# Kernel optimization log

Hardware: AMD Instinct MI355X
Metric: run time of the kernel (lower is better)

The kernel has to match this reference:

```python
import jax, jax.numpy as jnp
import numpy as np

HIDDEN = 3584
NUM_HEADS = 28
NUM_KV_HEADS = 4
HEAD_DIM = 128
ROPE_THETA = 1000000.0
B, S = 2, 2048


def setup_inputs() -> dict:
    key = jax.random.key(0)
    k1, k2, k3, k4 = jax.random.split(key, 4)
    q_size = NUM_HEADS * HEAD_DIM
    kv_size = NUM_KV_HEADS * HEAD_DIM
    return {
        "positions": jnp.arange(B * S, dtype=jnp.int32).reshape(B, S),
        "hidden_states": jax.random.normal(k1, (B, S, HIDDEN), dtype=jnp.float32),
        "w_qkv": jax.random.normal(k2, (HIDDEN, q_size + 2 * kv_size), dtype=jnp.float32) * (HIDDEN ** -0.5),
        "b_qkv": jax.random.normal(k3, (q_size + 2 * kv_size,), dtype=jnp.float32) * 0.02,
        "w_o": jax.random.normal(k4, (q_size, HIDDEN), dtype=jnp.float32) * (q_size ** -0.5),
    }


def _rope_cos_sin(positions):
    # NeoX-style rotary embedding, rotary_dim == head_dim
    half = HEAD_DIM // 2
    inv_freq = 1.0 / (ROPE_THETA ** (jnp.arange(0, half, dtype=jnp.float32) * 2.0 / HEAD_DIM))
    angles = positions.astype(jnp.float32)[..., None] * inv_freq  # [B, S, half]
    return jnp.cos(angles), jnp.sin(angles)


def _apply_rope(x, cos, sin):
    # x: [B, S, H, D]; cos/sin: [B, S, half] -> broadcast over heads
    x1, x2 = jnp.split(x, 2, axis=-1)
    c = cos[:, :, None, :]
    s = sin[:, :, None, :]
    return jnp.concatenate([x1 * c - x2 * s, x2 * c + x1 * s], axis=-1)


def reference(positions, hidden_states, w_qkv, b_qkv, w_o):
    q_size = NUM_HEADS * HEAD_DIM
    kv_size = NUM_KV_HEADS * HEAD_DIM
    scaling = HEAD_DIM ** -0.5
    groups = NUM_HEADS // NUM_KV_HEADS

    qkv = hidden_states @ w_qkv + b_qkv  # [B, S, q+2kv]
    q, k, v = jnp.split(qkv, [q_size, q_size + kv_size], axis=-1)
    q = q.reshape(B, S, NUM_HEADS, HEAD_DIM)
    k = k.reshape(B, S, NUM_KV_HEADS, HEAD_DIM)
    v = v.reshape(B, S, NUM_KV_HEADS, HEAD_DIM)

    cos, sin = _rope_cos_sin(positions)
    q = _apply_rope(q, cos, sin)
    k = _apply_rope(k, cos, sin)

    # GQA: group query heads over kv heads. q: [B, S, Hkv, G, D]
    qg = q.reshape(B, S, NUM_KV_HEADS, groups, HEAD_DIM)
    scores = jnp.einsum("bqhgd,bkhd->bhgqk", qg, k) * scaling  # [B, Hkv, G, S, S]
    causal = jnp.tril(jnp.ones((S, S), dtype=bool))
    scores = jnp.where(causal, scores, jnp.finfo(scores.dtype).min)
    probs = jax.nn.softmax(scores, axis=-1)
    o = jnp.einsum("bhgqk,bkhd->bqhgd", probs, v)  # [B, S, Hkv, G, D]
    o = o.reshape(B, S, NUM_HEADS * HEAD_DIM)
    return o @ w_o  # [B, S, HIDDEN]
```

## Files before the change

kernel.cpp:

```cpp
#include <hip/hip_runtime.h>

typedef unsigned short u16;
typedef unsigned int u32;
typedef __bf16 bf16x8 __attribute__((ext_vector_type(8)));
typedef float f32x4 __attribute__((ext_vector_type(4)));

#define NHEAD 28
#define NKVH 4
#define HD 128
#define NB 2
#define NS 2048
#define NTOK 4096
#define HIDDEN_DIM 3584
#define QKVW 4608
#define QSZ 3584
#define KOFF 3584
#define VOFF 4096
#define VSLAB (NTOK * 512)
#define QSCALE_L2E 0.12751744f

__device__ __forceinline__ float bf2f(u16 u) {
  u32 x = ((u32)u) << 16; float f; __builtin_memcpy(&f, &x, 4); return f;
}
__device__ __forceinline__ u16 f2bf(float f) {
  u32 x; __builtin_memcpy(&x, &f, 4);
  x += 0x7FFFu + ((x >> 16) & 1u);
  return (u16)(x >> 16);
}
__device__ __forceinline__ u32 pack2bf(float a, float b) {
  __bf16 lo = (__bf16)a, hi = (__bf16)b;
  u16 ul, uh;
  __builtin_memcpy(&ul, &lo, 2); __builtin_memcpy(&uh, &hi, 2);
  return (u32)ul | ((u32)uh << 16);
}
__device__ __forceinline__ void async16(const void* g, void* lds) {
  __builtin_amdgcn_global_load_lds((const __attribute__((address_space(1))) void*)g,
                                   (__attribute__((address_space(3))) void*)lds,
                                   16, 0, 0);
}

#define SB __builtin_amdgcn_sched_barrier(0)
#define BAR do { SB; __builtin_amdgcn_s_barrier(); SB; } while (0)

__global__ void cast_f32_bf16(const float* __restrict__ in, u16* __restrict__ out) {
  int i = (blockIdx.x * 256 + threadIdx.x) * 4;
  float4 v = *(const float4*)(in + i);
  u32 p0 = (u32)f2bf(v.x) | ((u32)f2bf(v.y) << 16);
  u32 p1 = (u32)f2bf(v.z) | ((u32)f2bf(v.w) << 16);
  uint2 r; r.x = p0; r.y = p1;
  *(uint2*)(out + i) = r;
}

__global__ void transpose_cast(const float* __restrict__ in, u16* __restrict__ out,
                               int R, int C) {
  __shared__ float tile[32][33];
  int tx = threadIdx.x & 31, ty = threadIdx.x >> 5;
  int c0 = blockIdx.x * 32, r0 = blockIdx.y * 32;
#pragma unroll
  for (int i = 0; i < 32; i += 8)
    tile[ty + i][tx] = in[(size_t)(r0 + ty + i) * C + c0 + tx];
  __syncthreads();
#pragma unroll
  for (int i = 0; i < 32; i += 8)
    out[(size_t)(c0 + ty + i) * R + r0 + tx] = f2bf(tile[tx][ty + i]);
}

__global__ void rope_table(const int* __restrict__ positions,
                           float* __restrict__ cs, float* __restrict__ sn) {
  int idx = blockIdx.x * 256 + threadIdx.x;
  int t = idx >> 6, i = idx & 63;
  float p = (float)positions[t];
  float inv = expf(-(float)i * (13.815510557964274f / 64.f));
  float a = p * inv;
  cs[idx] = cosf(a);
  sn[idx] = sinf(a);
}

__global__ void rope_kernel(u16* __restrict__ qkv, const float* __restrict__ cs,
                            const float* __restrict__ sn) {
  int w = threadIdx.x >> 6, l = threadIdx.x & 63;
  int rid = blockIdx.x * 4 + w;
  int t = rid >> 5, hh = rid & 31;
  size_t base = (size_t)t * QKVW + (hh < NHEAD ? hh * HD : KOFF + (hh - NHEAD) * HD);
  float x1 = bf2f(qkv[base + l]), x2 = bf2f(qkv[base + l + 64]);
  float c = cs[t * 64 + l], s = sn[t * 64 + l];
  float y1 = x1 * c - x2 * s;
  float y2 = x2 * c + x1 * s;
  if (hh < NHEAD) { y1 *= QSCALE_L2E; y2 *= QSCALE_L2E; }
  qkv[base + l] = f2bf(y1);
  qkv[base + l + 64] = f2bf(y2);
}

template <int MODE>
__global__ __launch_bounds__(512, 2) void gemm256(
    const u16* __restrict__ A, const u16* __restrict__ Bt,
    const float* __restrict__ bias, u16* __restrict__ outb,
    float* __restrict__ outf, int M, int Next, int Kst, int ldc, int NT) {
  __shared__ __align__(16) u16 Al[2][256 * 64];
  __shared__ __align__(16) u16 Bl[2][256 * 64];
  const int tid = threadIdx.x;
  const int l = tid & 63, w = tid >> 6;
  const int g = l >> 4, r = l & 15;
  const int wm = w >> 2, wn = w & 3;
  const int nbx = Next >> 8;
  const int cpx = (int)gridDim.x >> 3;
  const int bid = ((int)blockIdx.x & 7) * cpx + ((int)blockIdx.x >> 3);
  int bx, by, kbase;
  float* outp = outf;
  if (MODE == 2) {
    const int tps = nbx * (M >> 8);
    const int ks = bid / tps, rem = bid % tps;
    by = rem / nbx; bx = rem % nbx;
    kbase = ks * (NT << 6);
    outp = outf + (size_t)ks * M * Next;
  } else {
    bx = bid % nbx; by = bid / nbx; kbase = 0;
  }
  const int row0 = by * 256, col0 = bx * 256;

  f32x4 acc[8][4] = {};
  bf16x8 af[4][2];
  bf16x8 bfr[2][2][2];

  auto stageU = [&](const u16* mb, int base0, char* ldsMat, int h, int t) {
#pragma unroll
    for (int q = 0; q < 2; ++q) {
      const int idx = q * 512 + tid;
      const int rho = h * 128 + (idx >> 3);
      const int sl = (idx & 7) ^ (rho & 7);
      async16(mb + (size_t)(base0 + rho) * Kst + kbase + t * 64 + sl * 8,
              ldsMat + (size_t)(t & 1) * 32768 + h * 16384 + idx * 16);
    }
  };

#define READ_A(s, rh)                                                           \
  _Pragma("unroll") for (int fr = 0; fr < 4; ++fr) {                            \
    const int row_ = (rh) * 128 + wm * 64 + fr * 16 + r;                        \
    _Pragma("unroll") for (int kk = 0; kk < 2; ++kk) {                          \
      const int sl_ = (kk * 4 + g) ^ (row_ & 7);                                \
      af[fr][kk] = *(const bf16x8*)((const char*)Al + (s) * 32768 +             \
                                    row_ * 128 + sl_ * 16);                     \
    }                                                                           \
  }
#define READ_B(s, ch)                                                           \
  _Pragma("unroll") for (int fc = 0; fc < 2; ++fc) {                            \
    const int col_ = (ch) * 128 + wn * 32 + fc * 16 + r;                        \
    _Pragma("unroll") for (int kk = 0; kk < 2; ++kk) {                          \
      const int sl_ = (kk * 4 + g) ^ (col_ & 7);                                \
      bfr[ch][fc][kk] = *(const bf16x8*)((const char*)Bl + (s) * 32768 +        \
                                         col_ * 128 + sl_ * 16);                \
    }                                                                           \
  }
#define MFMA_Q(rh, ch)                                                          \
  __builtin_amdgcn_s_setprio(1);                                                \
  _Pragma("unroll") for (int fr = 0; fr < 4; ++fr)                              \
  _Pragma("unroll") for (int fc = 0; fc < 2; ++fc)                              \
  _Pragma("unroll") for (int kk = 0; kk < 2; ++kk)                              \
    acc[(rh) * 4 + fr][(ch) * 2 + fc] = __builtin_amdgcn_mfma_f32_16x16x32_bf16( \
        af[fr][kk], bfr[ch][fc][kk], acc[(rh) * 4 + fr][(ch) * 2 + fc], 0, 0, 0);\
  __builtin_amdgcn_s_setprio(0);

  stageU(A, row0, (char*)Al, 0, 0); stageU(A, row0, (char*)Al, 1, 0);
  stageU(Bt, col0, (char*)Bl, 0, 0); stageU(Bt, col0, (char*)Bl, 1, 0);
  stageU(A, row0, (char*)Al, 0, 1); stageU(Bt, col0, (char*)Bl, 0, 1);
  SB; asm volatile("s_waitcnt vmcnt(4)" ::: "memory");
  BAR;

  for (int t = 0; t < NT; ++t) {
    const int s = t & 1;
    READ_A(s, 0); READ_B(s, 0);
    if (t + 1 < NT) stageU(A, row0, (char*)Al, 1, t + 1);
    BAR; MFMA_Q(0, 0); BAR;
    READ_B(s, 1);
    if (t + 1 < NT) stageU(Bt, col0, (char*)Bl, 1, t + 1);
    BAR; MFMA_Q(0, 1); BAR;
    READ_A(s, 1);
    if (t + 2 < NT) stageU(A, row0, (char*)Al, 0, t + 2);
    BAR; MFMA_Q(1, 0); BAR;
    if (t + 2 < NT) stageU(Bt, col0, (char*)Bl, 0, t + 2);
    BAR; MFMA_Q(1, 1);
    if (t < NT - 2)        { SB; asm volatile("s_waitcnt vmcnt(4)" ::: "memory"); }
    else if (t == NT - 2)  { SB; asm volatile("s_waitcnt vmcnt(0)" ::: "memory"); }
    BAR;
  }
  SB; asm volatile("s_waitcnt vmcnt(0)" ::: "memory");

#pragma unroll
  for (int m = 0; m < 8; ++m) {
    const int row = row0 + (m >> 2) * 128 + wm * 64 + (m & 3) * 16 + g * 4;
#pragma unroll
    for (int n = 0; n < 4; ++n) {
      const int col = col0 + (n >> 1) * 128 + wn * 32 + (n & 1) * 16 + r;
      const float bb = (MODE == 0) ? bias[col] : 0.f;
#pragma unroll
      for (int j = 0; j < 4; ++j) {
        float v = acc[m][n][j] + bb;
        if (MODE == 0) outb[(size_t)(row + j) * ldc + col] = f2bf(v);
        else           outp[(size_t)(row + j) * ldc + col] = v;
      }
    }
  }
}

__global__ void v_reduce(const float* __restrict__ slabs, const float* __restrict__ bias,
                         u16* __restrict__ vtg) {
  __shared__ float tile[32][33];
  const int tx = threadIdx.x & 31, ty = threadIdx.x >> 5;
  const int c0 = blockIdx.x * 32;
  const int r0 = blockIdx.y * 32;
#pragma unroll
  for (int i = 0; i < 32; i += 8) {
    const size_t idx = (size_t)(r0 + ty + i) * 512 + c0 + tx;
    float s = slabs[idx] + slabs[idx + VSLAB] + slabs[idx + 2 * VSLAB] +
              slabs[idx + 3 * VSLAB];
    tile[ty + i][tx] = s + bias[VOFF + c0 + tx];
  }
  __syncthreads();
#pragma unroll
  for (int i = 0; i < 32; i += 8) {
    const int col = c0 + ty + i;
    const int row = r0 + tx;
    vtg[((size_t)((((row >> 11) * NKVH) + (col >> 7)) * HD + (col & 127))) * NS +
        (row & 2047)] = f2bf(tile[tx][ty + i]);
  }
}

__global__ __launch_bounds__(512) void attn_kernel(const u16* __restrict__ qkv,
                                                   const u16* __restrict__ vtg,
                                                   u16* __restrict__ Oh) {
  __shared__ __align__(16) u16 Ks[2][64 * 128];
  __shared__ __align__(16) u16 Vt[128 * 64];
  const int tid = threadIdx.x, l = tid & 63, w = tid >> 6;
  const int g = l >> 4, r = l & 15;
  const int bidx = blockIdx.x;
  const int qt = 15 - (bidx & 15);
  const int bh = bidx >> 4;
  const int h = bh % NHEAD, b = bh / NHEAD;
  const int kvh = h / 7;
  const int q0 = qt * 128;

  const int qrow = q0 + w * 16 + r;
  const size_t qbase = (size_t)(b * NS + qrow) * QKVW + h * HD;
  bf16x8 qf[4];
#pragma unroll
  for (int ks = 0; ks < 4; ++ks)
    qf[ks] = *(const bf16x8*)(qkv + qbase + ks * 32 + g * 8);

  const u16* kb0 = qkv + (size_t)(b * NS) * QKVW + KOFF + kvh * HD;
  const u16* vb0 = vtg + (size_t)((b * NKVH + kvh) * HD) * NS;

  f32x4 oacc[8] = {};
  float mrun = -1e30f, lrun = 0.f;

  const int nkv = 2 * qt + 2;

  auto stageK = [&](u16* kdst, int kv0) {
#pragma unroll
    for (int i = 0; i < 2; ++i) {
      const int li = (w * 2 + i) * 64 + l;
      const int rr = li >> 4, c = li & 15;
      async16(kb0 + (size_t)(kv0 + rr) * QKVW + ((c ^ (rr & 7)) << 3),
              (char*)kdst + (w * 2 + i) * 1024);
    }
  };
  auto stageV = [&](int kv0) {
#pragma unroll
    for (int i = 0; i < 2; ++i) {
      const int li = (w * 2 + i) * 64 + l;
      const int d = li >> 3, c = li & 7;
      async16(vb0 + (size_t)d * NS + kv0 + ((c ^ (d & 7)) << 3),
              (char*)Vt + (w * 2 + i) * 1024);
    }
  };

  stageK(Ks[0], 0);
  int cur = 0;
  const int srcA = r + ((l & 16) << 1);
  const int srcB = srcA + 16;
  const bool hi = (l & 32) != 0;

  for (int kvt = 0; kvt < nkv; ++kvt) {
    const int kv0 = kvt * 64;
    asm volatile("s_waitcnt vmcnt(0) lgkmcnt(0)" ::: "memory");
    __builtin_amdgcn_s_barrier();
    __builtin_amdgcn_sched_barrier(0);

    stageV(kv0);
    const bool haveNext = (kvt + 1 < nkv);
    if (haveNext) stageK(Ks[cur ^ 1], kv0 + 64);

    const bool active = kv0 <= q0 + w * 16 + 15;

    union { u32 wrd[4]; bf16x8 v; } pf[2];
    if (active) {
      f32x4 sacc[4] = {};
      const char* ksB = (const char*)Ks[cur];
      __builtin_amdgcn_s_setprio(1);
#pragma unroll
      for (int n = 0; n < 4; ++n) {
        const int key = n * 16 + r;
        const int sw = (key & 7) << 4;
#pragma unroll
        for (int ks = 0; ks < 4; ++ks) {
          bf16x8 kf = *(const bf16x8*)(ksB + key * 256 + ((ks * 64 + g * 16) ^ sw));
          sacc[n] = __builtin_amdgcn_mfma_f32_16x16x32_bf16(kf, qf[ks], sacc[n], 0, 0, 0);
        }
      }
      __builtin_amdgcn_s_setprio(0);
      if (kv0 + 63 > q0 + w * 16) {
#pragma unroll
        for (int n = 0; n < 4; ++n) {
          const int key_g = kv0 + n * 16 + g * 4;
#pragma unroll
          for (int j = 0; j < 4; ++j)
            if (key_g + j > qrow) sacc[n][j] = -1e30f;
        }
      }
      float mx = fmaxf(fmaxf(sacc[0][0], sacc[0][1]), fmaxf(sacc[0][2], sacc[0][3]));
#pragma unroll
      for (int n = 1; n < 4; ++n)
        mx = fmaxf(mx, fmaxf(fmaxf(sacc[n][0], sacc[n][1]), fmaxf(sacc[n][2], sacc[n][3])));
      mx = fmaxf(mx, __shfl_xor(mx, 16, 64));
      mx = fmaxf(mx, __shfl_xor(mx, 32, 64));
      if (!__all(mx <= mrun + 8.0f)) {
        const float mnew = fmaxf(mrun, mx);
        const float scale = __builtin_amdgcn_exp2f(mrun - mnew);
        mrun = mnew;
        lrun *= scale;
#pragma unroll
        for (int dt = 0; dt < 8; ++dt) oacc[dt] *= scale;
      }
      float sum = 0.f;
#pragma unroll
      for (int n = 0; n < 4; ++n)
#pragma unroll
        for (int j = 0; j < 4; ++j) {
          float p = __builtin_amdgcn_exp2f(sacc[n][j] - mrun);
          sacc[n][j] = p;
          sum += p;
        }
      sum += __shfl_xor(sum, 16, 64);
      sum += __shfl_xor(sum, 32, 64);
      lrun += sum;

      u32 pk[4][2];
#pragma unroll
      for (int n = 0; n < 4; ++n) {
        pk[n][0] = pack2bf(sacc[n][0], sacc[n][1]);
        pk[n][1] = pack2bf(sacc[n][2], sacc[n][3]);
      }
#pragma unroll
      for (int ks2 = 0; ks2 < 2; ++ks2) {
        const int n0 = 2 * ks2, n1 = 2 * ks2 + 1;
#pragma unroll
        for (int hh2 = 0; hh2 < 2; ++hh2) {
          u32 a0 = (u32)__shfl((int)pk[n0][hh2], srcA, 64);
          u32 a1 = (u32)__shfl((int)pk[n1][hh2], srcA, 64);
          pf[ks2].wrd[hh2] = hi ? a1 : a0;
          u32 b0 = (u32)__shfl((int)pk[n0][hh2], srcB, 64);
          u32 b1 = (u32)__shfl((int)pk[n1][hh2], srcB, 64);
          pf[ks2].wrd[2 + hh2] = hi ? b1 : b0;
        }
      }
    }

    if (haveNext) asm volatile("s_waitcnt vmcnt(2)" ::: "memory");
    else          asm volatile("s_waitcnt vmcnt(0)" ::: "memory");
    __builtin_amdgcn_s_barrier();
    __builtin_amdgcn_sched_barrier(0);
    if (active) {
      const char* vtB = (const char*)Vt;
      __builtin_amdgcn_s_setprio(1);
#pragma unroll
      for (int ks2 = 0; ks2 < 2; ++ks2) {
#pragma unroll
        for (int dt = 0; dt < 8; ++dt) {
          const int d = dt * 16 + r;
          bf16x8 vf = *(const bf16x8*)(vtB + d * 128 +
                                       ((ks2 * 64 + g * 16) ^ ((d & 7) << 4)));
          oacc[dt] = __builtin_amdgcn_mfma_f32_16x16x32_bf16(vf, pf[ks2].v, oacc[dt], 0, 0, 0);
        }
      }
      __builtin_amdgcn_s_setprio(0);
    }
    cur ^= 1;
  }

  const float inv = 1.f / lrun;
  const size_t obase = (size_t)(b * NS + qrow) * QSZ + h * HD;
#pragma unroll
  for (int dt = 0; dt < 8; ++dt) {
    uint2 r2;
    r2.x = pack2bf(oacc[dt][0] * inv, oacc[dt][1] * inv);
    r2.y = pack2bf(oacc[dt][2] * inv, oacc[dt][3] * inv);
    *(uint2*)(Oh + obase + dt * 16 + 4 * g) = r2;
  }
}

extern "C" void kernel_launch(void* const* d_in, const int* in_sizes, int n_in,
                              void* d_out, int out_size, void* d_ws, size_t ws_size,
                              hipStream_t stream) {
  const int* positions = (const int*)d_in[0];
  const float* hidden = (const float*)d_in[1];
  const float* w_qkv = (const float*)d_in[2];
  const float* b_qkv = (const float*)d_in[3];
  const float* w_o = (const float*)d_in[4];
  float* out = (float*)d_out;

  char* ws = (char*)d_ws;
  const size_t XB_OFF = 0;
  const size_t WQT_OFF = 29360128;
  const size_t QKV_OFF = WQT_OFF + 33030144;
  const size_t CS_OFF = QKV_OFF + 37748736;
  const size_t SN_OFF = CS_OFF + 1048576;
  const size_t WS_NEED = SN_OFF + 1048576;
  if (ws_size < WS_NEED) return;

  u16* Xb = (u16*)(ws + XB_OFF);
  u16* WoT = (u16*)(ws + XB_OFF);
  u16* WqT = (u16*)(ws + WQT_OFF);
  u16* Oh = (u16*)(ws + WQT_OFF);
  u16* qkvb = (u16*)(ws + QKV_OFF);
  float* cs = (float*)(ws + CS_OFF);
  float* sn = (float*)(ws + SN_OFF);
  u16* vtg = (u16*)d_out;
  float* vslabs = (float*)((char*)d_out + 4194304);

  cast_f32_bf16<<<14336, 256, 0, stream>>>(hidden, Xb);
  transpose_cast<<<dim3(QKVW / 32, HIDDEN_DIM / 32), 256, 0, stream>>>(w_qkv, WqT, HIDDEN_DIM, QKVW);
  rope_table<<<(NTOK * 64) / 256, 256, 0, stream>>>(positions, cs, sn);

  gemm256<0><<<256, 512, 0, stream>>>(
      Xb, WqT, b_qkv, qkvb, nullptr, NTOK, 4096, HIDDEN_DIM, QKVW, HIDDEN_DIM / 64);

  gemm256<2><<<128, 512, 0, stream>>>(
      Xb, WqT + (size_t)VOFF * HIDDEN_DIM, nullptr, nullptr, vslabs,
      NTOK, 512, HIDDEN_DIM, 512, HIDDEN_DIM / 64 / 4);

  v_reduce<<<dim3(512 / 32, NTOK / 32), 256, 0, stream>>>(vslabs, b_qkv, vtg);

  rope_kernel<<<(NTOK * 32) / 4, 256, 0, stream>>>(qkvb, cs, sn);

  transpose_cast<<<dim3(HIDDEN_DIM / 32, QSZ / 32), 256, 0, stream>>>(w_o, WoT, QSZ, HIDDEN_DIM);

  attn_kernel<<<NB * NHEAD * (NS / 128), 512, 0, stream>>>(qkvb, vtg, Oh);

  gemm256<1><<<(HIDDEN_DIM / 256) * (NTOK / 256), 512, 0, stream>>>(
      Oh, WoT, nullptr, nullptr, out, NTOK, HIDDEN_DIM, QSZ, HIDDEN_DIM, QSZ / 64);
}
```

Measured before the change: 494.0 us.

## Make attention a persistent kernel with atomic job queue, heaviest tiles first

Attention blocks become persistent workers that pull (q-tile, batch, head) jobs from a global atomic counter. Jobs are ordered longest causal tile first, which load-balances the triangular work across CUs. The counter is reset inside the rope_table kernel. The per-iteration row-sum shuffle reduction is deferred to the end of each job, and the max shuffles now run only when a rescale happens. This adds an atomic plus a block barrier per job. Reusing LDS across jobs relies on the existing barriers for ordering.

```diff
diff --git a/kernel.cpp b/kernel.cpp
--- a/kernel.cpp
+++ b/kernel.cpp
@@ -17,6 +17,8 @@
 #define KOFF 3584
 #define VOFF 4096
 #define VSLAB (NTOK * 512)
+#define NJOBS 896
+#define ATTN_BLOCKS 768
 #define QSCALE_L2E 0.12751744f
 
 __device__ __forceinline__ float bf2f(u16 u) {
@@ -66,7 +68,9 @@
 }
 
 __global__ void rope_table(const int* __restrict__ positions,
-                           float* __restrict__ cs, float* __restrict__ sn) {
+                           float* __restrict__ cs, float* __restrict__ sn,
+                           int* __restrict__ ctr) {
+  if (blockIdx.x == 0 && threadIdx.x == 0) *ctr = 0;
   int idx = blockIdx.x * 256 + threadIdx.x;
   int t = idx >> 6, i = idx & 63;
   float p = (float)positions[t];
@@ -227,173 +231,181 @@
 
 __global__ __launch_bounds__(512) void attn_kernel(const u16* __restrict__ qkv,
                                                    const u16* __restrict__ vtg,
-                                                   u16* __restrict__ Oh) {
+                                                   u16* __restrict__ Oh,
+                                                   int* __restrict__ ctr) {
   __shared__ __align__(16) u16 Ks[2][64 * 128];
   __shared__ __align__(16) u16 Vt[128 * 64];
+  __shared__ int s_job;
   const int tid = threadIdx.x, l = tid & 63, w = tid >> 6;
   const int g = l >> 4, r = l & 15;
-  const int bidx = blockIdx.x;
-  const int qt = 15 - (bidx & 15);
-  const int bh = bidx >> 4;
-  const int h = bh % NHEAD, b = bh / NHEAD;
-  const int kvh = h / 7;
-  const int q0 = qt * 128;
-
-  const int qrow = q0 + w * 16 + r;
-  const size_t qbase = (size_t)(b * NS + qrow) * QKVW + h * HD;
-  bf16x8 qf[4];
-#pragma unroll
-  for (int ks = 0; ks < 4; ++ks)
-    qf[ks] = *(const bf16x8*)(qkv + qbase + ks * 32 + g * 8);
-
-  const u16* kb0 = qkv + (size_t)(b * NS) * QKVW + KOFF + kvh * HD;
-  const u16* vb0 = vtg + (size_t)((b * NKVH + kvh) * HD) * NS;
-
-  f32x4 oacc[8] = {};
-  float mrun = -1e30f, lrun = 0.f;
-
-  const int nkv = 2 * qt + 2;
-
-  auto stageK = [&](u16* kdst, int kv0) {
-#pragma unroll
-    for (int i = 0; i < 2; ++i) {
-      const int li = (w * 2 + i) * 64 + l;
-      const int rr = li >> 4, c = li & 15;
-      async16(kb0 + (size_t)(kv0 + rr) * QKVW + ((c ^ (rr & 7)) << 3),
-              (char*)kdst + (w * 2 + i) * 1024);
-    }
-  };
-  auto stageV = [&](int kv0) {
-#pragma unroll
-    for (int i = 0; i < 2; ++i) {
-      const int li = (w * 2 + i) * 64 + l;
-      const int d = li >> 3, c = li & 7;
-      async16(vb0 + (size_t)d * NS + kv0 + ((c ^ (d & 7)) << 3),
-              (char*)Vt + (w * 2 + i) * 1024);
-    }
-  };
-
-  stageK(Ks[0], 0);
-  int cur = 0;
   const int srcA = r + ((l & 16) << 1);
   const int srcB = srcA + 16;
   const bool hi = (l & 32) != 0;
 
-  for (int kvt = 0; kvt < nkv; ++kvt) {
-    const int kv0 = kvt * 64;
-    asm volatile("s_waitcnt vmcnt(0) lgkmcnt(0)" ::: "memory");
-    __builtin_amdgcn_s_barrier();
-    __builtin_amdgcn_sched_barrier(0);
-
-    stageV(kv0);
-    const bool haveNext = (kvt + 1 < nkv);
-    if (haveNext) stageK(Ks[cur ^ 1], kv0 + 64);
-
-    const bool active = kv0 <= q0 + w * 16 + 15;
-
-    union { u32 wrd[4]; bf16x8 v; } pf[2];
-    if (active) {
-      f32x4 sacc[4] = {};
-      const char* ksB = (const char*)Ks[cur];
-      __builtin_amdgcn_s_setprio(1);
-#pragma unroll
-      for (int n = 0; n < 4; ++n) {
-        const int key = n * 16 + r;
-        const int sw = (key & 7) << 4;
-#pragma unroll
-        for (int ks = 0; ks < 4; ++ks) {
-          bf16x8 kf = *(const bf16x8*)(ksB + key * 256 + ((ks * 64 + g * 16) ^ sw));
-          sacc[n] = __builtin_amdgcn_mfma_f32_16x16x32_bf16(kf, qf[ks], sacc[n], 0, 0, 0);
-        }
+  for (;;) {
+    if (tid == 0) s_job = atomicAdd(ctr, 1);
+    __syncthreads();
+    const int jid = s_job;
+    if (jid >= NJOBS) return;
+    const int qtr = jid / 56;
+    const int qt = 15 - qtr;
+    const int bh = jid - qtr * 56;
+    const int h = bh % NHEAD, b = bh / NHEAD;
+    const int kvh = h / 7;
+    const int q0 = qt * 128;
+
+    const int qrow = q0 + w * 16 + r;
+    const size_t qbase = (size_t)(b * NS + qrow) * QKVW + h * HD;
+    bf16x8 qf[4];
+#pragma unroll
+    for (int ks = 0; ks < 4; ++ks)
+      qf[ks] = *(const bf16x8*)(qkv + qbase + ks * 32 + g * 8);
+
+    const u16* kb0 = qkv + (size_t)(b * NS) * QKVW + KOFF + kvh * HD;
+    const u16* vb0 = vtg + (size_t)((b * NKVH + kvh) * HD) * NS;
+
+    f32x4 oacc[8] = {};
+    float mrun = -1e30f, lsum = 0.f;
+
+    const int nkv = 2 * qt + 2;
+
+    auto stageK = [&](u16* kdst, int kv0) {
+#pragma unroll
+      for (int i = 0; i < 2; ++i) {
+        const int li = (w * 2 + i) * 64 + l;
+        const int rr = li >> 4, c = li & 15;
+        async16(kb0 + (size_t)(kv0 + rr) * QKVW + ((c ^ (rr & 7)) << 3),
+                (char*)kdst + (w * 2 + i) * 1024);
       }
-      __builtin_amdgcn_s_setprio(0);
-      if (kv0 + 63 > q0 + w * 16) {
+    };
+    auto stageV = [&](int kv0) {
+#pragma unroll
+      for (int i = 0; i < 2; ++i) {
+        const int li = (w * 2 + i) * 64 + l;
+        const int d = li >> 3, c = li & 7;
+        async16(vb0 + (size_t)d * NS + kv0 + ((c ^ (d & 7)) << 3),
+                (char*)Vt + (w * 2 + i) * 1024);
+      }
+    };
+
+    stageK(Ks[0], 0);
+    int cur = 0;
+
+    for (int kvt = 0; kvt < nkv; ++kvt) {
+      const int kv0 = kvt * 64;
+      asm volatile("s_waitcnt vmcnt(0) lgkmcnt(0)" ::: "memory");
+      __builtin_amdgcn_s_barrier();
+      __builtin_amdgcn_sched_barrier(0);
+
+      stageV(kv0);
+      const bool haveNext = (kvt + 1 < nkv);
+      if (haveNext) stageK(Ks[cur ^ 1], kv0 + 64);
+
+      const bool active = kv0 <= q0 + w * 16 + 15;
+
+      union { u32 wrd[4]; bf16x8 v; } pf[2];
+      if (active) {
+        f32x4 sacc[4] = {};
+        const char* ksB = (const char*)Ks[cur];
+        __builtin_amdgcn_s_setprio(1);
 #pragma unroll
         for (int n = 0; n < 4; ++n) {
-          const int key_g = kv0 + n * 16 + g * 4;
-#pragma unroll
-          for (int j = 0; j < 4; ++j)
-            if (key_g + j > qrow) sacc[n][j] = -1e30f;
+          const int key = n * 16 + r;
+          const int sw = (key & 7) << 4;
+#pragma unroll
+          for (int ks = 0; ks < 4; ++ks) {
+            bf16x8 kf = *(const bf16x8*)(ksB + key * 256 + ((ks * 64 + g * 16) ^ sw));
+            sacc[n] = __builtin_amdgcn_mfma_f32_16x16x32_bf16(kf, qf[ks], sacc[n], 0, 0, 0);
+          }
+        }
+        __builtin_amdgcn_s_setprio(0);
+        if (kv0 + 63 > q0 + w * 16) {
+#pragma unroll
+          for (int n = 0; n < 4; ++n) {
+            const int key_g = kv0 + n * 16 + g * 4;
+#pragma unroll
+            for (int j = 0; j < 4; ++j)
+              if (key_g + j > qrow) sacc[n][j] = -1e30f;
+          }
+        }
+        float mx = fmaxf(fmaxf(sacc[0][0], sacc[0][1]), fmaxf(sacc[0][2], sacc[0][3]));
+#pragma unroll
+        for (int n = 1; n < 4; ++n)
+          mx = fmaxf(mx, fmaxf(fmaxf(sacc[n][0], sacc[n][1]), fmaxf(sacc[n][2], sacc[n][3])));
+        if (!__all(mx <= mrun + 8.0f)) {
+          mx = fmaxf(mx, __shfl_xor(mx, 16, 64));
+          mx = fmaxf(mx, __shfl_xor(mx, 32, 64));
+          const float mnew = fmaxf(mrun, mx);
+          const float scale = __builtin_amdgcn_exp2f(mrun - mnew);
+          mrun = mnew;
+          lsum *= scale;
+#pragma unroll
+          for (int dt = 0; dt < 8; ++dt) oacc[dt] *= scale;
+        }
+#pragma unroll
+        for (int n = 0; n < 4; ++n)
+#pragma unroll
+          for (int j = 0; j < 4; ++j) {
+            float p = __builtin_amdgcn_exp2f(sacc[n][j] - mrun);
+            sacc[n][j] = p;
+            lsum += p;
+          }
+
+        u32 pk[4][2];
+#pragma unroll
+        for (int n = 0; n < 4; ++n) {
+          pk[n][0] = pack2bf(sacc[n][0], sacc[n][1]);
+          pk[n][1] = pack2bf(sacc[n][2], sacc[n][3]);
+        }
+#pragma unroll
+        for (int ks2 = 0; ks2 < 2; ++ks2) {
+          const int n0 = 2 * ks2, n1 = 2 * ks2 + 1;
+#pragma unroll
+          for (int hh2 = 0; hh2 < 2; ++hh2) {
+            u32 a0 = (u32)__shfl((int)pk[n0][hh2], srcA, 64);
+            u32 a1 = (u32)__shfl((int)pk[n1][hh2], srcA, 64);
+            pf[ks2].wrd[hh2] = hi ? a1 : a0;
+            u32 b0 = (u32)__shfl((int)pk[n0][hh2], srcB, 64);
+            u32 b1 = (u32)__shfl((int)pk[n1][hh2], srcB, 64);
+            pf[ks2].wrd[2 + hh2] = hi ? b1 : b0;
+          }
         }
       }
-      float mx = fmaxf(fmaxf(sacc[0][0], sacc[0][1]), fmaxf(sacc[0][2], sacc[0][3]));
-#pragma unroll
-      for (int n = 1; n < 4; ++n)
-        mx = fmaxf(mx, fmaxf(fmaxf(sacc[n][0], sacc[n][1]), fmaxf(sacc[n][2], sacc[n][3])));
-      mx = fmaxf(mx, __shfl_xor(mx, 16, 64));
-      mx = fmaxf(mx, __shfl_xor(mx, 32, 64));
-      if (!__all(mx <= mrun + 8.0f)) {
-        const float mnew = fmaxf(mrun, mx);
-        const float scale = __builtin_amdgcn_exp2f(mrun - mnew);
-        mrun = mnew;
-        lrun *= scale;
-#pragma unroll
-        for (int dt = 0; dt < 8; ++dt) oacc[dt] *= scale;
+
+      if (haveNext) asm volatile("s_waitcnt vmcnt(2)" ::: "memory");
+      else          asm volatile("s_waitcnt vmcnt(0)" ::: "memory");
+      __builtin_amdgcn_s_barrier();
+      __builtin_amdgcn_sched_barrier(0);
+      if (active) {
+        const char* vtB = (const char*)Vt;
+        __builtin_amdgcn_s_setprio(1);
+#pragma unroll
+        for (int ks2 = 0; ks2 < 2; ++ks2) {
+#pragma unroll
+          for (int dt = 0; dt < 8; ++dt) {
+            const int d = dt * 16 + r;
+            bf16x8 vf = *(const bf16x8*)(vtB + d * 128 +
+                                         ((ks2 * 64 + g * 16) ^ ((d & 7) << 4)));
+            oacc[dt] = __builtin_amdgcn_mfma_f32_16x16x32_bf16(vf, pf[ks2].v, oacc[dt], 0, 0, 0);
+          }
+        }
+        __builtin_amdgcn_s_setprio(0);
       }
-      float sum = 0.f;
-#pragma unroll
-      for (int n = 0; n < 4; ++n)
-#pragma unroll
-        for (int j = 0; j < 4; ++j) {
-          float p = __builtin_amdgcn_exp2f(sacc[n][j] - mrun);
-          sacc[n][j] = p;
-          sum += p;
-        }
-      sum += __shfl_xor(sum, 16, 64);
-      sum += __shfl_xor(sum, 32, 64);
-      lrun += sum;
-
-      u32 pk[4][2];
-#pragma unroll
-      for (int n = 0; n < 4; ++n) {
-        pk[n][0] = pack2bf(sacc[n][0], sacc[n][1]);
-        pk[n][1] = pack2bf(sacc[n][2], sacc[n][3]);
-      }
-#pragma unroll
-      for (int ks2 = 0; ks2 < 2; ++ks2) {
-        const int n0 = 2 * ks2, n1 = 2 * ks2 + 1;
-#pragma unroll
-        for (int hh2 = 0; hh2 < 2; ++hh2) {
-          u32 a0 = (u32)__shfl((int)pk[n0][hh2], srcA, 64);
-          u32 a1 = (u32)__shfl((int)pk[n1][hh2], srcA, 64);
-          pf[ks2].wrd[hh2] = hi ? a1 : a0;
-          u32 b0 = (u32)__shfl((int)pk[n0][hh2], srcB, 64);
-          u32 b1 = (u32)__shfl((int)pk[n1][hh2], srcB, 64);
-          pf[ks2].wrd[2 + hh2] = hi ? b1 : b0;
-        }
-      }
+      cur ^= 1;
     }
 
-    if (haveNext) asm volatile("s_waitcnt vmcnt(2)" ::: "memory");
-    else          asm volatile("s_waitcnt vmcnt(0)" ::: "memory");
-    __builtin_amdgcn_s_barrier();
-    __builtin_amdgcn_sched_barrier(0);
-    if (active) {
-      const char* vtB = (const char*)Vt;
-      __builtin_amdgcn_s_setprio(1);
-#pragma unroll
-      for (int ks2 = 0; ks2 < 2; ++ks2) {
-#pragma unroll
-        for (int dt = 0; dt < 8; ++dt) {
-          const int d = dt * 16 + r;
-          bf16x8 vf = *(const bf16x8*)(vtB + d * 128 +
-                                       ((ks2 * 64 + g * 16) ^ ((d & 7) << 4)));
-          oacc[dt] = __builtin_amdgcn_mfma_f32_16x16x32_bf16(vf, pf[ks2].v, oacc[dt], 0, 0, 0);
-        }
-      }
-      __builtin_amdgcn_s_setprio(0);
+    float lr = lsum;
+    lr += __shfl_xor(lr, 16, 64);
+    lr += __shfl_xor(lr, 32, 64);
+    const float inv = 1.f / lr;
+    const size_t obase = (size_t)(b * NS + qrow) * QSZ + h * HD;
+#pragma unroll
+    for (int dt = 0; dt < 8; ++dt) {
+      uint2 r2;
+      r2.x = pack2bf(oacc[dt][0] * inv, oacc[dt][1] * inv);
+      r2.y = pack2bf(oacc[dt][2] * inv, oacc[dt][3] * inv);
+      *(uint2*)(Oh + obase + dt * 16 + 4 * g) = r2;
     }
-    cur ^= 1;
-  }
-
-  const float inv = 1.f / lrun;
-  const size_t obase = (size_t)(b * NS + qrow) * QSZ + h * HD;
-#pragma unroll
-  for (int dt = 0; dt < 8; ++dt) {
-    uint2 r2;
-    r2.x = pack2bf(oacc[dt][0] * inv, oacc[dt][1] * inv);
-    r2.y = pack2bf(oacc[dt][2] * inv, oacc[dt][3] * inv);
-    *(uint2*)(Oh + obase + dt * 16 + 4 * g) = r2;
   }
 }
 
@@ -413,7 +425,8 @@
   const size_t QKV_OFF = WQT_OFF + 33030144;
   const size_t CS_OFF = QKV_OFF + 37748736;
   const size_t SN_OFF = CS_OFF + 1048576;
-  const size_t WS_NEED = SN_OFF + 1048576;
+  const size_t CTR_OFF = SN_OFF + 1048576;
+  const size_t WS_NEED = CTR_OFF + 64;
   if (ws_size < WS_NEED) return;
 
   u16* Xb = (u16*)(ws + XB_OFF);
@@ -423,12 +436,13 @@
   u16* qkvb = (u16*)(ws + QKV_OFF);
   float* cs = (float*)(ws + CS_OFF);
   float* sn = (float*)(ws + SN_OFF);
+  int* ctr = (int*)(ws + CTR_OFF);
   u16* vtg = (u16*)d_out;
   float* vslabs = (float*)((char*)d_out + 4194304);
 
   cast_f32_bf16<<<14336, 256, 0, stream>>>(hidden, Xb);
   transpose_cast<<<dim3(QKVW / 32, HIDDEN_DIM / 32), 256, 0, stream>>>(w_qkv, WqT, HIDDEN_DIM, QKVW);
-  rope_table<<<(NTOK * 64) / 256, 256, 0, stream>>>(positions, cs, sn);
+  rope_table<<<(NTOK * 64) / 256, 256, 0, stream>>>(positions, cs, sn, ctr);
 
   gemm256<0><<<256, 512, 0, stream>>>(
       Xb, WqT, b_qkv, qkvb, nullptr, NTOK, 4096, HIDDEN_DIM, QKVW, HIDDEN_DIM / 64);
@@ -443,7 +457,7 @@
 
   transpose_cast<<<dim3(HIDDEN_DIM / 32, QSZ / 32), 256, 0, stream>>>(w_o, WoT, QSZ, HIDDEN_DIM);
 
-  attn_kernel<<<NB * NHEAD * (NS / 128), 512, 0, stream>>>(qkvb, vtg, Oh);
+  attn_kernel<<<ATTN_BLOCKS, 512, 0, stream>>>(qkvb, vtg, Oh, ctr);
 
   gemm256<1><<<(HIDDEN_DIM / 256) * (NTOK / 256), 512, 0, stream>>>(
       Oh, WoT, nullptr, nullptr, out, NTOK, HIDDEN_DIM, QSZ, HIDDEN_DIM, QSZ / 64);
```

After: 446.3 us (median of 3 runs). -9.7%, faster.
